# Performance work log

Measured on AMD Instinct MI355X. Metric: run time of the kernel, lower is better.

## Reference

```python
import jax, jax.numpy as jnp
import numpy as np

N = 12288
IN_CH = 64
OUT_CH = 32


def setup_inputs() -> dict:
    key = jax.random.key(0)
    k_x, k_adj, k_w = jax.random.split(key, 3)
    x = jax.random.normal(k_x, (N, IN_CH), dtype=jnp.float32)
    # binary adjacency matrix (dense form of the sparse edge_index tensor)
    edge_index = jax.random.randint(k_adj, (N, N), 0, 2).astype(jnp.float32)
    # xavier_uniform for weight [in, out]
    limit = float(np.sqrt(6.0 / (IN_CH + OUT_CH)))
    weight = jax.random.uniform(k_w, (IN_CH, OUT_CH), dtype=jnp.float32,
                                minval=-limit, maxval=limit)
    bias = jnp.zeros((OUT_CH,), dtype=jnp.float32)
    return {"x": x, "edge_index": edge_index, "weight": weight, "bias": bias}


def reference(x, edge_index, weight, bias):
    # bgnn_a_norm: add self loops, then per-row norm = 1 / (rowsum^2 - sum(row^2))
    adj = edge_index + jnp.eye(edge_index.shape[0], dtype=edge_index.dtype)
    adj_sq = jnp.square(adj)
    row_sum = adj.sum(axis=-1)            # [N]
    denom = jnp.square(row_sum) - adj_sq.sum(axis=-1)  # [N]
    norm = 1.0 / denom
    norm = jnp.where(jnp.isinf(norm), 0.0, norm)       # [N]

    # bgnn_pool: (adj @ xw)^2 - adj^2 @ xw^2
    xw = x @ weight                        # [N, out]
    s = adj @ xw                           # [N, out]
    out = jnp.square(s) - adj_sq @ jnp.square(xw)

    # norm is a diagonal matrix in the original -> row-wise scale
    out = norm[:, None] * out + bias
    return out
```

## Files before the change

### kernel.cpp

```cpp
#include <hip/hip_runtime.h>


#define NN 12288
#define IN_CH 64
#define OUT_CH 32
#define KC 8
#define KPC (NN / KC)
#define NSTEP (KPC / 32)
#define MB 128
#define NMB (NN / MB)
#define NKSTEP (NN / 32)

typedef __attribute__((ext_vector_type(8))) short short8;
typedef __attribute__((ext_vector_type(4))) float f32x4;

static __device__ __forceinline__ unsigned short f2bf_rn(float f) {
    unsigned int u = __float_as_uint(f);
    u += 0x7fffu + ((u >> 16) & 1u);
    return (unsigned short)(u >> 16);
}

__global__ __launch_bounds__(256) void build_xw(const float* __restrict__ x,
                                                const float* __restrict__ w,
                                                float* __restrict__ XW) {
    int t = blockIdx.x * blockDim.x + threadIdx.x;
    int i = t >> 5;
    int c = t & 31;
    if (i >= NN) return;
    float acc = 0.f;
#pragma unroll
    for (int k4 = 0; k4 < IN_CH / 4; ++k4) {
        float4 xv = *(const float4*)&x[(size_t)i * IN_CH + k4 * 4];
        acc = fmaf(xv.x, w[(k4 * 4 + 0) * OUT_CH + c], acc);
        acc = fmaf(xv.y, w[(k4 * 4 + 1) * OUT_CH + c], acc);
        acc = fmaf(xv.z, w[(k4 * 4 + 2) * OUT_CH + c], acc);
        acc = fmaf(xv.w, w[(k4 * 4 + 3) * OUT_CH + c], acc);
    }
    XW[(size_t)i * OUT_CH + c] = acc;
}

__global__ __launch_bounds__(256) void packb(const float* __restrict__ XW,
                                             unsigned int* __restrict__ Bp) {
    int idx = blockIdx.x * 256 + threadIdx.x;
    int s = idx >> 9;
    int rem = idx & 511;
    int t = rem >> 6;
    int l = rem & 63;
    int kbase = s * 32 + ((l >> 4) * 8);
    int col = t * 16 + (l & 15);
    int cc = col & 31;
    bool sq = (col & 63) >= 32;
    bool lo = col >= 64;
    unsigned int out[4];
#pragma unroll
    for (int d = 0; d < 4; ++d) {
        unsigned short h[2];
#pragma unroll
        for (int j = 0; j < 2; ++j) {
            float v = XW[(size_t)(kbase + 2 * d + j) * OUT_CH + cc];
            if (sq) v *= v;
            unsigned short hb = f2bf_rn(v);
            if (lo) {
                float hf = __uint_as_float((unsigned int)hb << 16);
                hb = f2bf_rn(v - hf);
            }
            h[j] = hb;
        }
        out[d] = (unsigned int)h[0] | ((unsigned int)h[1] << 16);
    }
    *(uint4*)&Bp[(size_t)idx * 4] = *(uint4*)out;
}

__global__ __launch_bounds__(256) void spmm(const float* __restrict__ E,
                                            const unsigned int* __restrict__ Bp,
                                            float* __restrict__ S,
                                            float* __restrict__ RS) {
    const int mb = blockIdx.x % NMB;
    const int kc = blockIdx.x / NMB;
    const int tid = threadIdx.x;
    const int wid = tid >> 6;
    const int lane = tid & 63;
    const int r0 = mb * MB + wid * 32;
    const int row0 = r0 + (lane & 15);
    const int kq = (lane >> 4) * 8;

    f32x4 acc[2][8] = {};
    float rs[2] = {0.f, 0.f};

    const float* e0p = E + (size_t)row0 * NN + kc * KPC + kq;
    const float* e1p = e0p + (size_t)16 * NN;

    for (int s = 0; s < NSTEP; ++s) {
        const int koff = s * 32;
        float4 a0 = *(const float4*)(e0p + koff);
        float4 a1 = *(const float4*)(e0p + koff + 4);
        float4 c0 = *(const float4*)(e1p + koff);
        float4 c1 = *(const float4*)(e1p + koff + 4);

        const unsigned int* bp = Bp + (size_t)(kc * NSTEP + s) * 2048 + lane * 4;
        uint4 b[8];
#pragma unroll
        for (int t = 0; t < 8; ++t)
            b[t] = *(const uint4*)(bp + t * 256);

        union { unsigned int u[4]; short8 v; } pa, pb;
        pa.u[0] = (__float_as_uint(a0.x) >> 16) | (__float_as_uint(a0.y) & 0xffff0000u);
        pa.u[1] = (__float_as_uint(a0.z) >> 16) | (__float_as_uint(a0.w) & 0xffff0000u);
        pa.u[2] = (__float_as_uint(a1.x) >> 16) | (__float_as_uint(a1.y) & 0xffff0000u);
        pa.u[3] = (__float_as_uint(a1.z) >> 16) | (__float_as_uint(a1.w) & 0xffff0000u);
        pb.u[0] = (__float_as_uint(c0.x) >> 16) | (__float_as_uint(c0.y) & 0xffff0000u);
        pb.u[1] = (__float_as_uint(c0.z) >> 16) | (__float_as_uint(c0.w) & 0xffff0000u);
        pb.u[2] = (__float_as_uint(c1.x) >> 16) | (__float_as_uint(c1.y) & 0xffff0000u);
        pb.u[3] = (__float_as_uint(c1.z) >> 16) | (__float_as_uint(c1.w) & 0xffff0000u);

        rs[0] += ((a0.x + a0.y) + (a0.z + a0.w)) + ((a1.x + a1.y) + (a1.z + a1.w));
        rs[1] += ((c0.x + c0.y) + (c0.z + c0.w)) + ((c1.x + c1.y) + (c1.z + c1.w));

#pragma unroll
        for (int t = 0; t < 8; ++t) {
            union { uint4 q; short8 v; } bu;
            bu.q = b[t];
            acc[0][t] = __builtin_amdgcn_mfma_f32_16x16x32_bf16(pa.v, bu.v, acc[0][t], 0, 0, 0);
            acc[1][t] = __builtin_amdgcn_mfma_f32_16x16x32_bf16(pb.v, bu.v, acc[1][t], 0, 0, 0);
        }
    }

#pragma unroll
    for (int m = 0; m < 2; ++m) {
        float v = rs[m];
        v += __shfl_xor(v, 16, 64);
        v += __shfl_xor(v, 32, 64);
        if ((lane >> 4) == 0)
            atomicAdd(&RS[r0 + m * 16 + (lane & 15)], v);
    }

#pragma unroll
    for (int m = 0; m < 2; ++m) {
        const int rowb = r0 + m * 16 + (lane >> 4) * 4;
#pragma unroll
        for (int t = 0; t < 4; ++t) {
#pragma unroll
            for (int r = 0; r < 4; ++r) {
                float v = acc[m][t][r] + acc[m][t + 4][r];
                atomicAdd(&S[(size_t)(rowb + r) * 64 + t * 16 + (lane & 15)], v);
            }
        }
    }
}

__global__ __launch_bounds__(256) void epi(const float* __restrict__ E,
                                           const float* __restrict__ XW,
                                           const float* __restrict__ S,
                                           const float* __restrict__ RS,
                                           const float* __restrict__ bias,
                                           float* __restrict__ out) {
    int t = blockIdx.x * blockDim.x + threadIdx.x;
    int i = t >> 5;
    int c = t & 31;
    if (i >= NN) return;
    const float eii = E[(size_t)i * NN + i];
    const float xwc = XW[(size_t)i * OUT_CH + c];
    const float xw2c = xwc * xwc;
    const float s = S[(size_t)i * 64 + c] + xwc;
    const float tt = S[(size_t)i * 64 + 32 + c] + (eii != 0.f ? 3.f : 1.f) * xw2c;
    const float rse = RS[i];
    const float rsa = rse + 1.f;
    const float d1 = eii + 1.f;
    const float sumsq = rse - eii + d1 * d1;
    const float denom = rsa * rsa - sumsq;
    const float nrm = (denom == 0.f) ? 0.f : 1.f / denom;
    out[(size_t)i * OUT_CH + c] = nrm * (s * s - tt) + bias[c];
}

extern "C" void kernel_launch(void* const* d_in, const int* in_sizes, int n_in,
                              void* d_out, int out_size, void* d_ws, size_t ws_size,
                              hipStream_t stream) {
    const float* x    = (const float*)d_in[0];
    const float* E    = (const float*)d_in[1];
    const float* w    = (const float*)d_in[2];
    const float* bias = (const float*)d_in[3];
    float* out = (float*)d_out;

    float* XW = (float*)d_ws;
    unsigned int* Bp = (unsigned int*)(XW + (size_t)NN * OUT_CH);
    float* S = (float*)(Bp + (size_t)NKSTEP * 512 * 4);
    float* RS = S + (size_t)NN * 64;

    hipMemsetAsync(S, 0, ((size_t)NN * 64 + NN) * sizeof(float), stream);

    build_xw<<<NN * OUT_CH / 256, 256, 0, stream>>>(x, w, XW);
    packb<<<NKSTEP * 512 / 256, 256, 0, stream>>>(XW, Bp);
    spmm<<<NMB * KC, 256, 0, stream>>>(E, Bp, S, RS);
    epi<<<NN * OUT_CH / 256, 256, 0, stream>>>(E, XW, S, RS, bias, out);
}
```

Before: 818.4 us.

## Replace split-K atomics with per-slice partial buffers and nontemporal adjacency loads

The split-K spmm kernel now writes its per-chunk partial sums and row sums into dedicated slice buffers in MFMA fragment layout, and the epilogue reduces the eight slices itself. This removes the global atomicAdds and the memset of the accumulation buffer. Adjacency loads also become nontemporal so the streamed dense matrix does not pollute the cache. The cost is extra workspace and more scattered reads in the epilogue.

```diff
diff --git a/kernel.cpp b/kernel.cpp
--- a/kernel.cpp
+++ b/kernel.cpp
@@ -30,7 +30,7 @@
     float acc = 0.f;
 #pragma unroll
     for (int k4 = 0; k4 < IN_CH / 4; ++k4) {
-        float4 xv = *(const float4*)&x[(size_t)i * IN_CH + k4 * 4];
+        f32x4 xv = *(const f32x4*)&x[(size_t)i * IN_CH + k4 * 4];
         acc = fmaf(xv.x, w[(k4 * 4 + 0) * OUT_CH + c], acc);
         acc = fmaf(xv.y, w[(k4 * 4 + 1) * OUT_CH + c], acc);
         acc = fmaf(xv.z, w[(k4 * 4 + 2) * OUT_CH + c], acc);
@@ -73,8 +73,8 @@
 
 __global__ __launch_bounds__(256) void spmm(const float* __restrict__ E,
                                             const unsigned int* __restrict__ Bp,
-                                            float* __restrict__ S,
-                                            float* __restrict__ RS) {
+                                            float* __restrict__ Ssl,
+                                            float* __restrict__ RSsl) {
     const int mb = blockIdx.x % NMB;
     const int kc = blockIdx.x / NMB;
     const int tid = threadIdx.x;
@@ -92,10 +92,10 @@
 
     for (int s = 0; s < NSTEP; ++s) {
         const int koff = s * 32;
-        float4 a0 = *(const float4*)(e0p + koff);
-        float4 a1 = *(const float4*)(e0p + koff + 4);
-        float4 c0 = *(const float4*)(e1p + koff);
-        float4 c1 = *(const float4*)(e1p + koff + 4);
+        f32x4 a0 = __builtin_nontemporal_load((const f32x4*)(e0p + koff));
+        f32x4 a1 = __builtin_nontemporal_load((const f32x4*)(e0p + koff) + 1);
+        f32x4 c0 = __builtin_nontemporal_load((const f32x4*)(e1p + koff));
+        f32x4 c1 = __builtin_nontemporal_load((const f32x4*)(e1p + koff) + 1);
 
         const unsigned int* bp = Bp + (size_t)(kc * NSTEP + s) * 2048 + lane * 4;
         uint4 b[8];
@@ -131,45 +131,55 @@
         v += __shfl_xor(v, 16, 64);
         v += __shfl_xor(v, 32, 64);
         if ((lane >> 4) == 0)
-            atomicAdd(&RS[r0 + m * 16 + (lane & 15)], v);
-    }
-
+            RSsl[(size_t)kc * NN + r0 + m * 16 + (lane & 15)] = v;
+    }
+
+    const size_t sbase = (((size_t)kc * NMB + mb) * 4 + wid) * 2;
 #pragma unroll
     for (int m = 0; m < 2; ++m) {
-        const int rowb = r0 + m * 16 + (lane >> 4) * 4;
 #pragma unroll
         for (int t = 0; t < 4; ++t) {
-#pragma unroll
-            for (int r = 0; r < 4; ++r) {
-                float v = acc[m][t][r] + acc[m][t + 4][r];
-                atomicAdd(&S[(size_t)(rowb + r) * 64 + t * 16 + (lane & 15)], v);
-            }
+            f32x4 v = acc[m][t] + acc[m][t + 4];
+            *(f32x4*)&Ssl[((sbase + m) * 4 + t) * 256 + lane * 4] = v;
         }
     }
 }
 
 __global__ __launch_bounds__(256) void epi(const float* __restrict__ E,
                                            const float* __restrict__ XW,
-                                           const float* __restrict__ S,
-                                           const float* __restrict__ RS,
+                                           const float* __restrict__ Ssl,
+                                           const float* __restrict__ RSsl,
                                            const float* __restrict__ bias,
                                            float* __restrict__ out) {
-    int t = blockIdx.x * blockDim.x + threadIdx.x;
-    int i = t >> 5;
-    int c = t & 31;
+    int tt0 = blockIdx.x * blockDim.x + threadIdx.x;
+    int i = tt0 >> 5;
+    int c = tt0 & 31;
     if (i >= NN) return;
+    const int mb = i >> 7;
+    const int wid = (i >> 5) & 3;
+    const int m = (i >> 4) & 1;
+    const int lane_s = ((i >> 2) & 3) * 16 + (c & 15);
+    const int r = i & 3;
+    const int ts = c >> 4;
+    float s = 0.f, tsum = 0.f, rse = 0.f;
+#pragma unroll
+    for (int kc = 0; kc < KC; ++kc) {
+        const size_t base = ((((size_t)kc * NMB + mb) * 4 + wid) * 2 + m) * 4;
+        s    += Ssl[(base + ts) * 256 + lane_s * 4 + r];
+        tsum += Ssl[(base + 2 + ts) * 256 + lane_s * 4 + r];
+        rse  += RSsl[(size_t)kc * NN + i];
+    }
     const float eii = E[(size_t)i * NN + i];
     const float xwc = XW[(size_t)i * OUT_CH + c];
     const float xw2c = xwc * xwc;
-    const float s = S[(size_t)i * 64 + c] + xwc;
-    const float tt = S[(size_t)i * 64 + 32 + c] + (eii != 0.f ? 3.f : 1.f) * xw2c;
-    const float rse = RS[i];
+    s += xwc;
+    tsum += (eii != 0.f ? 3.f : 1.f) * xw2c;
     const float rsa = rse + 1.f;
     const float d1 = eii + 1.f;
     const float sumsq = rse - eii + d1 * d1;
     const float denom = rsa * rsa - sumsq;
     const float nrm = (denom == 0.f) ? 0.f : 1.f / denom;
-    out[(size_t)i * OUT_CH + c] = nrm * (s * s - tt) + bias[c];
+    out[(size_t)i * OUT_CH + c] = nrm * (s * s - tsum) + bias[c];
 }
 
 extern "C" void kernel_launch(void* const* d_in, const int* in_sizes, int n_in,
@@ -183,13 +193,11 @@
 
     float* XW = (float*)d_ws;
     unsigned int* Bp = (unsigned int*)(XW + (size_t)NN * OUT_CH);
-    float* S = (float*)(Bp + (size_t)NKSTEP * 512 * 4);
-    float* RS = S + (size_t)NN * 64;
-
-    hipMemsetAsync(S, 0, ((size_t)NN * 64 + NN) * sizeof(float), stream);
+    float* Ssl = (float*)(Bp + (size_t)NKSTEP * 512 * 4);
+    float* RSsl = Ssl + (size_t)KC * NMB * 4 * 2 * 4 * 256;
 
     build_xw<<<NN * OUT_CH / 256, 256, 0, stream>>>(x, w, XW);
     packb<<<NKSTEP * 512 / 256, 256, 0, stream>>>(XW, Bp);
-    spmm<<<NMB * KC, 256, 0, stream>>>(E, Bp, S, RS);
-    epi<<<NN * OUT_CH / 256, 256, 0, stream>>>(E, XW, S, RS, bias, out);
-}
+    spmm<<<NMB * KC, 256, 0, stream>>>(E, Bp, Ssl, RSsl);
+    epi<<<NN * OUT_CH / 256, 256, 0, stream>>>(E, XW, Ssl, RSsl, bias, out);
+}
```

Measured after the change: 836.3 us. +2.2%, slower.
